# Performance work log

Measured on AMD Instinct MI355X. Metric: run time of the kernel, lower is better.

## Reference

```python
import jax, jax.numpy as jnp
import numpy as np

B, P, G = 16, 4096, 512          # images, proposals/image, gt boxes/image
NUM_CLASSES = 80
IOU_THRESH = 0.5                  # cfg.MODEL.ROI_HEADS.IOU_THRESHOLDS = [0.5]
BATCH_PER_IMG = 512               # cfg.MODEL.ROI_HEADS.BATCH_SIZE_PER_IMAGE
POS_FRAC = 0.25                   # cfg.MODEL.ROI_HEADS.POSITIVE_FRACTION
NUM_FG = int(BATCH_PER_IMG * POS_FRAC)   # 128
NUM_BG = BATCH_PER_IMG - NUM_FG          # 384
NEG_INF = jnp.float32(-1e9)


def _make_boxes(key, b, n, img_size=1024.0):
    # valid xyxy boxes inside an img_size x img_size image
    p = jax.random.uniform(key, (b, n, 4)) * img_size
    x1 = jnp.minimum(p[..., 0], p[..., 2]); x2 = jnp.maximum(p[..., 0], p[..., 2]) + 1.0
    y1 = jnp.minimum(p[..., 1], p[..., 3]); y2 = jnp.maximum(p[..., 1], p[..., 3]) + 1.0
    return jnp.stack([x1, y1, x2, y2], axis=-1)


def setup_inputs() -> dict:
    key = jax.random.key(0)
    k1, k2, k3, k4 = jax.random.split(key, 4)
    return {
        'proposal_boxes': _make_boxes(k1, B, P),
        'target_boxes': _make_boxes(k2, B, G),
        'gt_classes': jax.random.randint(k3, (B, G), 0, NUM_CLASSES),
        'priorities': jax.random.uniform(k4, (B, P)),  # random sampling keys (replaces tf random subsample)
    }


def _pairwise_iou(t, p):
    # t: [B,G,4] gt boxes, p: [B,P,4] proposals, xyxy -> iou [B,G,P]
    area_t = (t[..., 2] - t[..., 0]) * (t[..., 3] - t[..., 1])   # [B,G]
    area_p = (p[..., 2] - p[..., 0]) * (p[..., 3] - p[..., 1])   # [B,P]
    lt = jnp.maximum(t[:, :, None, :2], p[:, None, :, :2])       # [B,G,P,2]
    rb = jnp.minimum(t[:, :, None, 2:], p[:, None, :, 2:])       # [B,G,P,2]
    wh = jnp.clip(rb - lt, 0.0)
    inter = wh[..., 0] * wh[..., 1]                               # [B,G,P]
    union = area_t[:, :, None] + area_p[:, None, :] - inter
    return jnp.where(inter > 0, inter / jnp.maximum(union, 1e-8), 0.0)


def reference(proposal_boxes, target_boxes, gt_classes, priorities):
    # ---- Matcher: pairwise IoU + argmax over gt (thresholds [0.5], labels [0,1]) ----
    iou = _pairwise_iou(target_boxes, proposal_boxes)       # [B,G,P]
    matched_vals = iou.max(axis=1)                          # [B,P]
    matched_idxs = iou.argmax(axis=1)                       # [B,P]
    fg = matched_vals >= IOU_THRESH                         # label==1
    # gt_classes per proposal: matched class if fg, else background = num_classes
    cls_m = jnp.take_along_axis(gt_classes, matched_idxs, axis=1)
    prop_cls = jnp.where(fg, cls_m, NUM_CLASSES)            # [B,P]
    # ---- subsample_labels: pick up to NUM_FG fg and NUM_BG bg by random priority ----
    fg_sc = jnp.where(fg, priorities, NEG_INF)
    bg_sc = jnp.where(~fg, priorities, NEG_INF)
    fg_v, fg_i = jax.lax.top_k(fg_sc, NUM_FG)               # [B,NUM_FG]
    bg_v, bg_i = jax.lax.top_k(bg_sc, NUM_BG)               # [B,NUM_BG]
    inds = jnp.concatenate([fg_i, bg_i], axis=1)            # [B,S]
    valid = jnp.concatenate([fg_v, bg_v], axis=1) > NEG_INF / 2
    # ---- gather sampled proposals + assigned gt (pad_or_clip: zero invalid slots) ----
    s_boxes = jnp.take_along_axis(proposal_boxes, inds[..., None], axis=1)   # [B,S,4]
    s_midx = jnp.take_along_axis(matched_idxs, inds, axis=1)                  # [B,S]
    s_gt_boxes = jnp.take_along_axis(target_boxes, s_midx[..., None], axis=1) # [B,S,4]
    s_cls = jnp.where(valid, jnp.take_along_axis(prop_cls, inds, axis=1), -1) # [B,S]
    mask = valid[..., None].astype(s_boxes.dtype)
    out = jnp.concatenate([s_boxes, s_gt_boxes], axis=-1) * mask              # [B,S,8]
    return out, s_cls
```

## Files before the change

kernel.cpp:

```cpp
#include <hip/hip_runtime.h>
#include <stdint.h>

#define NB 16
#define NP 4096
#define NG 512
#define NCH 8
#define GC  (NG/NCH)
#define NCLS 80
#define KFG 128
#define KBG 384
#define NS 512
#define OUT_BOX (NB*NS*8)
#define OUT_CLS (NB*NS)
#define NBNP (NB*NP)
#define NBK 256
#define NGRP (2*NBK)
#define RBLK 16
#define CHK (NP/RBLK)

typedef unsigned long long u64;

__global__ __launch_bounds__(256) void k_match(
    const float4* __restrict__ prop,
    const float4* __restrict__ tgt,
    u64* __restrict__ pm,
    float* __restrict__ out)
{
    const int tid  = threadIdx.x;
    const int bx   = blockIdx.x;
    const int c    = bx & (NCH - 1);
    const int pblk = (bx >> 3) & 15;
    const int b    = bx >> 7;

    const int gid = bx * 256 + tid;
    if (gid < OUT_BOX) out[gid] = 0.0f;
    if (gid < OUT_CLS) out[OUT_BOX + gid] = -1.0f;

    const int p = pblk * 256 + tid;
    const float4 pb = prop[b * NP + p];
    const float ap = __fmul_rn(__fsub_rn(pb.z, pb.x), __fsub_rn(pb.w, pb.y));

    const float4* __restrict__ tg = tgt + b * NG + c * GC;

    float best = -1.0f;
    int   bi   = 0;
    #pragma unroll 8
    for (int g = 0; g < GC; ++g) {
        const float4 t = tg[g];
        const float at  = __fmul_rn(__fsub_rn(t.z, t.x), __fsub_rn(t.w, t.y));
        const float ltx = fmaxf(t.x, pb.x);
        const float lty = fmaxf(t.y, pb.y);
        const float rbx = fminf(t.z, pb.z);
        const float rby = fminf(t.w, pb.w);
        const float w = fmaxf(__fsub_rn(rbx, ltx), 0.0f);
        const float h = fmaxf(__fsub_rn(rby, lty), 0.0f);
        const float inter = __fmul_rn(w, h);
        const float uni   = __fsub_rn(__fadd_rn(at, ap), inter);
        const float iou   = __fdiv_rn(inter, fmaxf(uni, 1e-8f));
        if (iou > best) { best = iou; bi = g; }
    }
    const int gg = c * GC + bi;
    pm[c * NBNP + b * NP + p] =
        ((u64)__float_as_uint(best) << 16) | (u64)(NG - 1 - gg);
}

__global__ __launch_bounds__(256) void k_combine(
    const float* __restrict__ pri,
    const u64*  __restrict__ pm,
    u64* __restrict__ pmc)
{
    const int idx = blockIdx.x * 256 + threadIdx.x;
    u64 m = pm[idx];
    #pragma unroll
    for (int c = 1; c < NCH; ++c) {
        const u64 mc = pm[c * NBNP + idx];
        if (mc > m) m = mc;
    }
    const float best = __uint_as_float((unsigned)(m >> 16));
    const int   mi   = (NG - 1) - (int)(m & 0xFFFF);
    const int   cat  = (best >= 0.5f) ? 1 : 0;
    const float v    = pri[idx];
    int bkt = (int)(v * 256.0f); if (bkt > 255) bkt = 255;
    pmc[idx] = ((u64)__float_as_uint(v) << 18) | ((u64)cat << 17)
             | ((u64)bkt << 9) | (u64)mi;
}

__global__ __launch_bounds__(512) void k_rank(
    const float4* __restrict__ prop,
    const float4* __restrict__ tgt,
    const int*   __restrict__ gtc,
    const float* __restrict__ pri,
    const u64*   __restrict__ pmc,
    float* __restrict__ out)
{
    __shared__ u64 gkeys[NP];
    __shared__ unsigned smeta[NP];
    __shared__ int cnt[NGRP];
    __shared__ int bsa[NGRP];
    __shared__ int cur[NGRP];
    __shared__ int sA[NGRP], sB[NGRP];
    __shared__ int s_tot0;

    const int tid = threadIdx.x;
    const int b   = blockIdx.x >> 4;
    const int j   = blockIdx.x & (RBLK - 1);

    cnt[tid] = 0;
    __syncthreads();

    u64 scmb[8];
    #pragma unroll
    for (int t = 0; t < 8; ++t) {
        const int p = tid + t * 512;
        const u64 cmb = pmc[b * NP + p];
        scmb[t] = cmb;
        smeta[p] = (unsigned)(cmb & 0x3FFFFu);
        atomicAdd(&cnt[(int)((cmb >> 9) & 0x1FF)], 1);
    }
    __syncthreads();

    sA[tid] = cnt[(tid & 256) | (255 - (tid & 255))];
    __syncthreads();

    int* pa = sA; int* pb2 = sB;
    for (int d = 1; d < NGRP; d <<= 1) {
        pb2[tid] = pa[tid] + ((tid >= d) ? pa[tid - d] : 0);
        __syncthreads();
        int* tmp = pa; pa = pb2; pb2 = tmp;
    }
    if (tid == 0) s_tot0 = pa[NBK - 1];
    {
        const int grp = (tid & 256) | (255 - (tid & 255));
        const int excl = pa[tid] - cnt[grp];
        bsa[grp] = excl;
        cur[grp] = excl;
    }
    __syncthreads();

    const int tot0 = s_tot0;

    #pragma unroll
    for (int t = 0; t < 8; ++t) {
        const u64 cmb = scmb[t];
        const int grp = (int)((cmb >> 9) & 0x1FF);
        const int cat = (int)((cmb >> 17) & 1);
        const int gs  = bsa[grp];
        const int cap = cat ? KFG : KBG;
        if (gs - (cat ? tot0 : 0) < cap) {
            const int p = tid + t * 512;
            const u64 key = ((cmb >> 18) << 12) | (u64)(NP - 1 - p);
            const int off = atomicAdd(&cur[grp], 1);
            gkeys[off] = key;
        }
    }
    __syncthreads();

    if (tid < CHK) {
        const int p   = j * CHK + tid;
        const int idx = b * NP + p;
        const unsigned meta = smeta[p];
        const int mi  = (int)(meta & 0x1FF);
        const int cat = (int)((meta >> 17) & 1);
        const int grp = (int)((meta >> 9) & 0x1FF);
        const int gs  = bsa[grp];
        const int catbase = cat ? tot0 : 0;
        const int cap = cat ? KFG : KBG;
        if (gs - catbase < cap) {
            const u64 mine = ((u64)__float_as_uint(pri[idx]) << 12)
                           | (u64)(NP - 1 - p);
            const int gc = cnt[grp];
            int ahead = 0;
            for (int i = gs; i < gs + gc; ++i)
                ahead += (gkeys[i] > mine) ? 1 : 0;
            const int rank = (gs - catbase) + ahead;
            if (rank < cap) {
                const int slot = b * NS + (cat ? rank : KFG + rank);
                const float4 pb4 = prop[idx];
                const float4 tb4 = tgt[b * NG + mi];
                float4* orow = (float4*)(out + (size_t)slot * 8);
                orow[0] = pb4;
                orow[1] = tb4;
                out[OUT_BOX + slot] = cat ? (float)gtc[b * NG + mi]
                                          : (float)NCLS;
            }
        }
    }
}

extern "C" void kernel_launch(void* const* d_in, const int* in_sizes, int n_in,
                              void* d_out, int out_size, void* d_ws, size_t ws_size,
                              hipStream_t stream) {
    const float4* prop = (const float4*)d_in[0];
    const float4* tgt  = (const float4*)d_in[1];
    const int*    gtc  = (const int*)  d_in[2];
    const float*  pri  = (const float*)d_in[3];
    float* out = (float*)d_out;

    u64* pm  = (u64*)d_ws;
    u64* pmc = (u64*)((char*)d_ws + (size_t)NCH * NBNP * 8);

    k_match<<<NB * 16 * NCH, 256, 0, stream>>>(prop, tgt, pm, out);
    k_combine<<<NBNP / 256, 256, 0, stream>>>(pri, pm, pmc);
    k_rank<<<NB * RBLK, 512, 0, stream>>>(prop, tgt, gtc, pri, pmc, out);
}
```

Measured before the change: 45.38 us.

## Replace per-pair IoU division with cross-multiplied comparison and exact fallback

The matching loop no longer divides for every gt/proposal pair. It compares candidate IoUs by cross-multiplying inter*bestUnion against bestInter*union, using FMA error terms and a relative threshold. If any comparison is too close to call, the thread reruns the original exact division loop so the argmax and tie-breaking stay bit-exact. This removes the correctly rounded division from the hot loop, at the cost of extra FMAs per pair and a divergent fallback path.

```diff
diff --git a/kernel.cpp b/kernel.cpp
--- a/kernel.cpp
+++ b/kernel.cpp
@@ -42,8 +42,9 @@
 
     const float4* __restrict__ tg = tgt + b * NG + c * GC;
 
-    float best = -1.0f;
-    int   bi   = 0;
+    float bA = -1.0f, bB = 1.0f;
+    int   bi  = 0;
+    bool  amb = false;
     #pragma unroll 8
     for (int g = 0; g < GC; ++g) {
         const float4 t = tg[g];
@@ -56,9 +57,41 @@
         const float h = fmaxf(__fsub_rn(rby, lty), 0.0f);
         const float inter = __fmul_rn(w, h);
         const float uni   = __fsub_rn(__fadd_rn(at, ap), inter);
-        const float iou   = __fdiv_rn(inter, fmaxf(uni, 1e-8f));
-        if (iou > best) { best = iou; bi = g; }
-    }
+
+        const float p1 = __fmul_rn(inter, bB);
+        const float e1 = fmaf(inter, bB, -p1);
+        const float p2 = __fmul_rn(bA, uni);
+        const float e2 = fmaf(bA, uni, -p2);
+        const float d  = __fsub_rn(p1, p2);
+        const float dd = __fadd_rn(d, __fsub_rn(e1, e2));
+        const float thr = __fmul_rn(fmaxf(p1, p2), 0x1p-20f);
+
+        const bool exact_tie = (d == 0.0f) & (e1 == e2);
+        amb = amb | ((__builtin_fabsf(dd) <= thr) & !exact_tie);
+        if (dd > thr) { bA = inter; bB = uni; bi = g; }
+    }
+
+    float best;
+    if (amb) {
+        best = -1.0f; bi = 0;
+        for (int g = 0; g < GC; ++g) {
+            const float4 t = tg[g];
+            const float at  = __fmul_rn(__fsub_rn(t.z, t.x), __fsub_rn(t.w, t.y));
+            const float ltx = fmaxf(t.x, pb.x);
+            const float lty = fmaxf(t.y, pb.y);
+            const float rbx = fminf(t.z, pb.z);
+            const float rby = fminf(t.w, pb.w);
+            const float w = fmaxf(__fsub_rn(rbx, ltx), 0.0f);
+            const float h = fmaxf(__fsub_rn(rby, lty), 0.0f);
+            const float inter = __fmul_rn(w, h);
+            const float uni   = __fsub_rn(__fadd_rn(at, ap), inter);
+            const float iou   = __fdiv_rn(inter, fmaxf(uni, 1e-8f));
+            if (iou > best) { best = iou; bi = g; }
+        }
+    } else {
+        best = __fdiv_rn(bA, fmaxf(bB, 1e-8f));
+    }
+
     const int gg = c * GC + bi;
     pm[c * NBNP + b * NP + p] =
         ((u64)__float_as_uint(best) << 16) | (u64)(NG - 1 - gg);
```

New measurement: 44.40 us. -2.1%, faster.
